# Kernel optimization log

Measured on AMD Instinct MI355X. Metric: run time of the kernel, lower is better.

Reference implementation:

```python
import jax, jax.numpy as jnp
import numpy as np

B, C, H, W = 32, 256, 64, 64
AS = 8  # attn_size


def _avgpool(x, s):
    # exact adaptive avg pool when H,W divisible by s: mean over each block
    b, c, h, w = x.shape
    return x.reshape(b, c, s, h // s, s, w // s).mean(axis=(3, 5))


def setup_inputs() -> dict:
    key = jax.random.key(0)
    ks = jax.random.split(key, 6)
    scale = 1.0 / np.sqrt(C)
    return {
        "F_rgb": jax.random.normal(ks[0], (B, C, H, W), jnp.float32),
        "F_d": jax.random.normal(ks[1], (B, C, H, W), jnp.float32),
        "Wq": jax.random.normal(ks[2], (C, C), jnp.float32) * scale,
        "bq": jnp.zeros((C,), jnp.float32),
        "Wk": jax.random.normal(ks[3], (C, C), jnp.float32) * scale,
        "bk": jnp.zeros((C,), jnp.float32),
        "Wv": jax.random.normal(ks[4], (C, C), jnp.float32) * scale,
        "bv": jnp.zeros((C,), jnp.float32),
        "alpha": jnp.float32(0.5),
    }


def reference(F_rgb, F_d, Wq, bq, Wk, bk, Wv, bv, alpha):
    b, c, h_in, w_in = F_rgb.shape
    R = _avgpool(F_rgb, AS)  # [B,C,8,8]
    D = _avgpool(F_d, AS)    # [B,C,8,8]
    # 1x1 convs == channel-mixing matmuls
    Q = jnp.einsum('oc,bchw->bohw', Wq, R) + bq[None, :, None, None]
    K = jnp.einsum('oc,bchw->bohw', Wk, D) + bk[None, :, None, None]
    V = jnp.einsum('oc,bchw->bohw', Wv, D) + bv[None, :, None, None]
    T = AS * AS
    Qf = Q.reshape(b, c, T)
    Kf = K.reshape(b, c, T)
    Vf = V.reshape(b, c, T)
    A = jnp.einsum('bct,bcs->bts', Qf, Kf)        # [B,T,T]
    A = jax.nn.softmax(A, axis=-1)
    Fatt = jnp.einsum('bcs,bts->bct', Vf, A)      # V @ A^T
    Fatt = Fatt.reshape(b, c, AS, AS)
    # bilinear upsample, half-pixel centers (== torch align_corners=False)
    Fatt = jax.image.resize(Fatt, (b, c, h_in, w_in), method='bilinear')
    return alpha * Fatt + (1.0 - alpha) * F_rgb
```

## Files before the change

### kernel.cpp

```cpp
#include <hip/hip_runtime.h>
#include <math.h>

#define B_  32
#define C_  256
#define T_  64
#define HW_ 4096

__global__ __launch_bounds__(256) void k_pool(const float* __restrict__ Frgb,
                                              const float* __restrict__ Fd,
                                              float* __restrict__ R,
                                              float* __restrict__ D) {
    __shared__ float s[128];
    const int tid = threadIdx.x;
    const int plane = blockIdx.x;
    if (tid < 128) s[tid] = 0.f;
    __syncthreads();
    const float4* pr = (const float4*)Frgb + (size_t)plane * 1024;
    const float4* pd = (const float4*)Fd   + (size_t)plane * 1024;
    const int cellx = (tid & 15) >> 1;
    const int hbit  = tid >> 7;
    #pragma unroll
    for (int k = 0; k < 4; ++k) {
        const int cell = (2*k + hbit) * 8 + cellx;
        float4 a = pr[k*256 + tid];
        atomicAdd(&s[cell], a.x + a.y + a.z + a.w);
        float4 b = pd[k*256 + tid];
        atomicAdd(&s[64 + cell], b.x + b.y + b.z + b.w);
    }
    __syncthreads();
    if (tid < 64)        R[(size_t)plane*64 + tid]        = s[tid]      * (1.f/64.f);
    else if (tid < 128)  D[(size_t)plane*64 + (tid - 64)] = s[tid]      * (1.f/64.f);
}

__global__ __launch_bounds__(256) void k_qkv(const float* __restrict__ R, const float* __restrict__ D,
                                             const float* __restrict__ Wq, const float* __restrict__ bq,
                                             const float* __restrict__ Wk, const float* __restrict__ bk,
                                             const float* __restrict__ Wv, const float* __restrict__ bv,
                                             float* __restrict__ Q, float* __restrict__ K,
                                             float* __restrict__ V) {
    __shared__ float Ws[32 * 256];
    const int tid = threadIdx.x;
    const int tbase = blockIdx.x * 16;
    const int b = blockIdx.y;
    const int z = blockIdx.z;
    const float* W    = (z == 0) ? Wq : (z == 1) ? Wk : Wv;
    const float* bias = (z == 0) ? bq : (z == 1) ? bk : bv;
    const float* X    = (z == 0) ? R  : D;
    float* Out        = (z == 0) ? Q  : (z == 1) ? K  : V;

    const int o = tid;
    float acc[16];
    const float bz = bias[o];
    #pragma unroll
    for (int t = 0; t < 16; ++t) acc[t] = bz;

    const float* Xb = X + (size_t)b * C_ * T_;
    for (int cb = 0; cb < 256; cb += 32) {
        __syncthreads();
        #pragma unroll
        for (int k = 0; k < 8; ++k) {
            float4 w4 = *(const float4*)(W + (size_t)o * 256 + cb + k*4);
            Ws[(k*4 + 0)*256 + o] = w4.x;
            Ws[(k*4 + 1)*256 + o] = w4.y;
            Ws[(k*4 + 2)*256 + o] = w4.z;
            Ws[(k*4 + 3)*256 + o] = w4.w;
        }
        __syncthreads();
        for (int cl = 0; cl < 32; ++cl) {
            const float w = Ws[cl*256 + o];
            const float* xrow = Xb + (size_t)(cb + cl) * T_ + tbase;
            #pragma unroll
            for (int t = 0; t < 16; ++t) acc[t] += w * xrow[t];
        }
    }
    float* orow = Out + ((size_t)b * C_ + o) * T_ + tbase;
    #pragma unroll
    for (int t = 0; t < 16; ++t) orow[t] = acc[t];
}

__global__ __launch_bounds__(256) void k_attn(const float* __restrict__ Q,
                                              const float* __restrict__ K,
                                              const float* __restrict__ V,
                                              float* __restrict__ Fatt) {
    __shared__ float Ks[128 * 64];
    __shared__ float As[64 * 65];
    const int tid  = threadIdx.x;
    const int lane = tid & 63;
    const int wv   = __builtin_amdgcn_readfirstlane(tid >> 6);
    const int b = blockIdx.x;

    float acc[16];
    #pragma unroll
    for (int t = 0; t < 16; ++t) acc[t] = 0.f;

    const float* Qb = Q + (size_t)b * C_ * T_;
    const float* Kb = K + (size_t)b * C_ * T_;
    for (int half = 0; half < 2; ++half) {
        __syncthreads();
        const float4* src = (const float4*)(Kb + half * 128 * 64);
        float4* dst = (float4*)Ks;
        #pragma unroll
        for (int k = 0; k < 8; ++k) dst[k*256 + tid] = src[k*256 + tid];
        __syncthreads();
        for (int cl = 0; cl < 128; ++cl) {
            const float kv = Ks[cl*64 + lane];
            const float* qrow = Qb + (size_t)(half*128 + cl) * T_ + wv*16;
            #pragma unroll
            for (int t = 0; t < 16; ++t) acc[t] += kv * qrow[t];
        }
    }

    #pragma unroll
    for (int t = 0; t < 16; ++t) {
        float m = acc[t];
        #pragma unroll
        for (int off = 32; off; off >>= 1) m = fmaxf(m, __shfl_xor(m, off));
        const float e = __expf(acc[t] - m);
        float ssum = e;
        #pragma unroll
        for (int off = 32; off; off >>= 1) ssum += __shfl_xor(ssum, off);
        As[lane*65 + wv*16 + t] = e / ssum;
    }
    __syncthreads();

    float av[64];
    #pragma unroll
    for (int s = 0; s < 64; ++s) av[s] = As[s*65 + lane];
    const float* Vb = V + (size_t)b * C_ * T_;
    float* Fb = Fatt + (size_t)b * C_ * T_;
    for (int cc = 0; cc < 64; ++cc) {
        const int c = wv*64 + cc;
        const float* vrow = Vb + (size_t)c * T_;
        float sum = 0.f;
        #pragma unroll
        for (int s = 0; s < 64; ++s) sum = fmaf(vrow[s], av[s], sum);
        Fb[(size_t)c * T_ + lane] = sum;
    }
}

__global__ __launch_bounds__(256) void k_up(const float* __restrict__ Fatt,
                                            const float* __restrict__ Frgb,
                                            const float* __restrict__ alphap,
                                            float* __restrict__ Out) {
    __shared__ float Fs[64];
    const int tid = threadIdx.x;
    const int plane = blockIdx.x;
    if (tid < 64) Fs[tid] = Fatt[(size_t)plane*64 + tid];
    __syncthreads();
    const float alpha = alphap[0];
    const float beta = 1.f - alpha;
    const float4* rgb4 = (const float4*)Frgb + (size_t)plane * 1024;
    float4* out4 = (float4*)Out + (size_t)plane * 1024;
    #pragma unroll
    for (int k = 0; k < 4; ++k) {
        const int flat = k*1024 + tid*4;
        const int y  = flat >> 6;
        const int xb = flat & 63;
        const float sy = y * 0.125f - 0.4375f;
        const float fy = floorf(sy);
        const float wy = sy - fy;
        const int iy = (int)fy;
        const int y0 = iy < 0 ? 0 : iy;
        const int y1 = (iy + 1) > 7 ? 7 : (iy + 1);
        float4 rv = rgb4[k*256 + tid];
        float o[4];
        const float rs[4] = {rv.x, rv.y, rv.z, rv.w};
        #pragma unroll
        for (int j = 0; j < 4; ++j) {
            const int x = xb + j;
            const float sx = x * 0.125f - 0.4375f;
            const float fx = floorf(sx);
            const float wx = sx - fx;
            const int ix = (int)fx;
            const int x0 = ix < 0 ? 0 : ix;
            const int x1 = (ix + 1) > 7 ? 7 : (ix + 1);
            const float top = (1.f - wx) * Fs[y0*8 + x0] + wx * Fs[y0*8 + x1];
            const float bot = (1.f - wx) * Fs[y1*8 + x0] + wx * Fs[y1*8 + x1];
            const float v = (1.f - wy) * top + wy * bot;
            o[j] = alpha * v + beta * rs[j];
        }
        out4[k*256 + tid] = make_float4(o[0], o[1], o[2], o[3]);
    }
}

extern "C" void kernel_launch(void* const* d_in, const int* in_sizes, int n_in,
                              void* d_out, int out_size, void* d_ws, size_t ws_size,
                              hipStream_t stream) {
    const float* Frgb  = (const float*)d_in[0];
    const float* Fd    = (const float*)d_in[1];
    const float* Wq    = (const float*)d_in[2];
    const float* bq    = (const float*)d_in[3];
    const float* Wk    = (const float*)d_in[4];
    const float* bk    = (const float*)d_in[5];
    const float* Wv    = (const float*)d_in[6];
    const float* bv    = (const float*)d_in[7];
    const float* alpha = (const float*)d_in[8];

    float* ws = (float*)d_ws;
    const size_t PC = (size_t)B_ * C_ * T_;
    float* R    = ws;
    float* D    = ws + PC;
    float* Q    = ws + 2*PC;
    float* K    = ws + 3*PC;
    float* V    = ws + 4*PC;
    float* Fatt = ws + 5*PC;
    float* Out  = (float*)d_out;

    k_pool<<<B_*C_, 256, 0, stream>>>(Frgb, Fd, R, D);
    k_qkv <<<dim3(4, 32, 3), 256, 0, stream>>>(R, D, Wq, bq, Wk, bk, Wv, bv, Q, K, V);
    k_attn<<<B_, 256, 0, stream>>>(Q, K, V, Fatt);
    k_up  <<<B_*C_, 256, 0, stream>>>(Fatt, Frgb, alpha, Out);
}
```

Measured before the change: 480.8 us.

## Move V@A^T into upsample kernel and replace pool atomics with shared-memory reduction

The attention kernel now only computes the softmax matrix and writes it transposed to workspace. The V-times-A^T product moves into the per-plane upsample kernel, spreading that work across 8192 blocks instead of 32 blocks of serial channel loops. The pool kernel stores per-thread partial sums in shared memory and reduces them per cell instead of using shared atomics. The cost is an extra A matrix read per plane, which should mostly hit cache, and more shared memory in the pool kernel.

```diff
diff --git a/kernel.cpp b/kernel.cpp
--- a/kernel.cpp
+++ b/kernel.cpp
@@ -10,26 +10,31 @@
                                               const float* __restrict__ Fd,
                                               float* __restrict__ R,
                                               float* __restrict__ D) {
-    __shared__ float s[128];
+    __shared__ float P[2][1024];
     const int tid = threadIdx.x;
     const int plane = blockIdx.x;
-    if (tid < 128) s[tid] = 0.f;
-    __syncthreads();
     const float4* pr = (const float4*)Frgb + (size_t)plane * 1024;
     const float4* pd = (const float4*)Fd   + (size_t)plane * 1024;
-    const int cellx = (tid & 15) >> 1;
-    const int hbit  = tid >> 7;
     #pragma unroll
     for (int k = 0; k < 4; ++k) {
-        const int cell = (2*k + hbit) * 8 + cellx;
         float4 a = pr[k*256 + tid];
-        atomicAdd(&s[cell], a.x + a.y + a.z + a.w);
+        P[0][k*256 + tid] = a.x + a.y + a.z + a.w;
         float4 b = pd[k*256 + tid];
-        atomicAdd(&s[64 + cell], b.x + b.y + b.z + b.w);
-    }
-    __syncthreads();
-    if (tid < 64)        R[(size_t)plane*64 + tid]        = s[tid]      * (1.f/64.f);
-    else if (tid < 128)  D[(size_t)plane*64 + (tid - 64)] = s[tid]      * (1.f/64.f);
+        P[1][k*256 + tid] = b.x + b.y + b.z + b.w;
+    }
+    __syncthreads();
+    if (tid < 128) {
+        const int tensor = tid >> 6;
+        const int cell = tid & 63;
+        const int cy = cell >> 3, cx = cell & 7;
+        const int base = (cy >> 1)*256 + (cy & 1)*128 + 2*cx;
+        float s = 0.f;
+        #pragma unroll
+        for (int rg = 0; rg < 8; ++rg)
+            s += P[tensor][base + rg*16] + P[tensor][base + rg*16 + 1];
+        float* dst = tensor ? D : R;
+        dst[(size_t)plane*64 + cell] = s * (1.f/64.f);
+    }
 }
 
 __global__ __launch_bounds__(256) void k_qkv(const float* __restrict__ R, const float* __restrict__ D,
@@ -78,10 +83,9 @@
     for (int t = 0; t < 16; ++t) orow[t] = acc[t];
 }
 
-__global__ __launch_bounds__(256) void k_attn(const float* __restrict__ Q,
-                                              const float* __restrict__ K,
-                                              const float* __restrict__ V,
-                                              float* __restrict__ Fatt) {
+__global__ __launch_bounds__(256) void k_attnA(const float* __restrict__ Q,
+                                               const float* __restrict__ K,
+                                               float* __restrict__ AT) {
     __shared__ float Ks[128 * 64];
     __shared__ float As[64 * 65];
     const int tid  = threadIdx.x;
@@ -123,30 +127,44 @@
     }
     __syncthreads();
 
-    float av[64];
-    #pragma unroll
-    for (int s = 0; s < 64; ++s) av[s] = As[s*65 + lane];
-    const float* Vb = V + (size_t)b * C_ * T_;
-    float* Fb = Fatt + (size_t)b * C_ * T_;
-    for (int cc = 0; cc < 64; ++cc) {
-        const int c = wv*64 + cc;
-        const float* vrow = Vb + (size_t)c * T_;
-        float sum = 0.f;
-        #pragma unroll
-        for (int s = 0; s < 64; ++s) sum = fmaf(vrow[s], av[s], sum);
-        Fb[(size_t)c * T_ + lane] = sum;
-    }
-}
-
-__global__ __launch_bounds__(256) void k_up(const float* __restrict__ Fatt,
+    float* ATb = AT + (size_t)b * T_ * T_;
+    #pragma unroll
+    for (int i = 0; i < 16; ++i) {
+        const int idx = i*256 + tid;
+        const int s = idx >> 6, t = idx & 63;
+        ATb[idx] = As[s*65 + t];
+    }
+}
+
+__global__ __launch_bounds__(256) void k_up(const float* __restrict__ AT,
+                                            const float* __restrict__ V,
                                             const float* __restrict__ Frgb,
                                             const float* __restrict__ alphap,
                                             float* __restrict__ Out) {
+    __shared__ float Vs[64];
+    __shared__ float Ps[4][64];
     __shared__ float Fs[64];
     const int tid = threadIdx.x;
     const int plane = blockIdx.x;
-    if (tid < 64) Fs[tid] = Fatt[(size_t)plane*64 + tid];
-    __syncthreads();
+    const int b = plane >> 8;
+    if (tid < 64) Vs[tid] = V[(size_t)plane*64 + tid];
+    __syncthreads();
+    {
+        const int t = tid & 63;
+        const int sq = tid >> 6;
+        const float* ATb = AT + (size_t)b * T_ * T_;
+        float sum = 0.f;
+        #pragma unroll
+        for (int j = 0; j < 16; ++j) {
+            const int s = sq*16 + j;
+            sum = fmaf(Vs[s], ATb[s*64 + t], sum);
+        }
+        Ps[sq][t] = sum;
+    }
+    __syncthreads();
+    if (tid < 64) Fs[tid] = Ps[0][tid] + Ps[1][tid] + Ps[2][tid] + Ps[3][tid];
+    __syncthreads();
+
     const float alpha = alphap[0];
     const float beta = 1.f - alpha;
     const float4* rgb4 = (const float4*)Frgb + (size_t)plane * 1024;
@@ -203,11 +221,11 @@
     float* Q    = ws + 2*PC;
     float* K    = ws + 3*PC;
     float* V    = ws + 4*PC;
-    float* Fatt = ws + 5*PC;
+    float* AT   = ws + 5*PC;
     float* Out  = (float*)d_out;
 
-    k_pool<<<B_*C_, 256, 0, stream>>>(Frgb, Fd, R, D);
-    k_qkv <<<dim3(4, 32, 3), 256, 0, stream>>>(R, D, Wq, bq, Wk, bk, Wv, bv, Q, K, V);
-    k_attn<<<B_, 256, 0, stream>>>(Q, K, V, Fatt);
-    k_up  <<<B_*C_, 256, 0, stream>>>(Fatt, Frgb, alpha, Out);
-}
+    k_pool <<<B_*C_, 256, 0, stream>>>(Frgb, Fd, R, D);
+    k_qkv  <<<dim3(4, 32, 3), 256, 0, stream>>>(R, D, Wq, bq, Wk, bk, Wv, bv, Q, K, V);
+    k_attnA<<<B_, 256, 0, stream>>>(Q, K, AT);
+    k_up   <<<B_*C_, 256, 0, stream>>>(AT, V, Frgb, alpha, Out);
+}
```

New measurement: 418.8 us. -12.9%, faster.
